# Kernel tuning notes

Hardware: AMD Instinct MI355X
Metric: run time of the kernel (lower is better)

## Reference

```python
import jax, jax.numpy as jnp
import numpy as np
from jax import lax

B, T, IN, H = 128, 1024, 130, 512


def setup_inputs() -> dict:
    key = jax.random.key(0)
    ks = jax.random.split(key, 6)
    inputs = jax.random.normal(ks[0], (B, T, IN), dtype=jnp.float32)
    # valid lengths in [1, T] (forward indexes outputs[len-1])
    inputs_len = jax.random.randint(ks[1], (B,), 1, T + 1)
    h0 = jnp.zeros((B, H), dtype=jnp.float32)
    c0 = jnp.zeros((B, H), dtype=jnp.float32)
    s = 1.0 / np.sqrt(H)
    W_ih = jax.random.uniform(ks[2], (4 * H, IN - 2), jnp.float32, -s, s)
    W_hh = jax.random.uniform(ks[3], (4 * H, H), jnp.float32, -s, s)
    b_ih = jax.random.uniform(ks[4], (4 * H,), jnp.float32, -s, s)
    b_hh = jax.random.uniform(ks[5], (4 * H,), jnp.float32, -s, s)
    return {"inputs": inputs, "inputs_len": inputs_len, "h0": h0, "c0": c0,
            "W_ih": W_ih, "W_hh": W_hh, "b_ih": b_ih, "b_hh": b_hh}


def _lstm_encode(inputs, h0, c0, W_ih, W_hh, b_ih, b_hh):
    # drop last 2 features (coordinates), as in stard_LSTM branch
    x = inputs[..., :-2]                                   # [B, T, IN-2]
    # precompute input projections for all timesteps (same math as per-step)
    xproj = jnp.einsum('bti,gi->tbg', x, W_ih) + b_ih + b_hh  # [T, B, 4H]

    def step(carry, xw):
        h, c = carry
        gates = xw + h @ W_hh.T                            # [B, 4H]
        i, f, g, o = jnp.split(gates, 4, axis=-1)
        i = jax.nn.sigmoid(i)
        f = jax.nn.sigmoid(f)
        g = jnp.tanh(g)
        o = jax.nn.sigmoid(o)
        c2 = f * c + i * g
        h2 = o * jnp.tanh(c2)
        return (h2, c2), h2

    _, hs = lax.scan(step, (h0, c0), xproj)                # hs: [T, B, H]
    return hs


def reference(inputs, inputs_len, h0, c0, W_ih, W_hh, b_ih, b_hh):
    hs = _lstm_encode(inputs, h0, c0, W_ih, W_hh, b_ih, b_hh)
    # gather hidden state at last valid timestep per sequence
    b_idx = jnp.arange(inputs.shape[0])
    return hs[inputs_len - 1, b_idx]                       # [B, H]
```

## Files before the change

### kernel.cpp

```cpp
#include <hip/hip_runtime.h>
#include <hip/hip_bf16.h>
#include <cstdint>
#include <cstddef>

#define T_STEPS 1024
#define BATCH   128
#define INF     128
#define HID     512
#define NBLK    256
#define NTHR    512
#define PK      648
#define Z_SHORTS    (2 * 16 * PK)
#define GSTR        17
#define GATE_FLOATS (4 * 4 * 16 * GSTR)
#define SMEM_BYTES  (Z_SHORTS * 2 + GATE_FLOATS * 4)

typedef short  bf16x8 __attribute__((ext_vector_type(8)));
typedef float  f32x4  __attribute__((ext_vector_type(4)));

static __device__ __forceinline__ unsigned short bf_hi(float v) {
  __hip_bfloat16 h = __float2bfloat16(v);
  return *reinterpret_cast<unsigned short*>(&h);
}
static __device__ __forceinline__ float bf_val(unsigned short u) {
  __hip_bfloat16 h = *reinterpret_cast<__hip_bfloat16*>(&u);
  return __bfloat162float(h);
}
static __device__ __forceinline__ float fsigmoid(float x) {
  return 1.f / (1.f + __expf(-x));
}
static __device__ __forceinline__ float ftanh(float x) {
  return 1.f - 2.f / (__expf(2.f * x) + 1.f);
}


__global__ __launch_bounds__(256) void k_prep_x(const float* __restrict__ in,
                                                unsigned short* __restrict__ xp)
{
  int t = blockIdx.x >> 3, bg = blockIdx.x & 7;
  int tid = threadIdx.x;
  size_t base = (size_t)blockIdx.x * 4096;
  #pragma unroll
  for (int rep = 0; rep < 8; ++rep) {
    int idx = rep * 256 + tid;
    int c = idx >> 7, k = idx & 127;
    float v = in[((size_t)(bg * 16 + c) * T_STEPS + t) * 130 + k];
    unsigned short hi = bf_hi(v);
    unsigned short lo = bf_hi(v - bf_val(hi));
    xp[base + c * 128 + k]        = hi;
    xp[base + 2048 + c * 128 + k] = lo;
  }
}

__global__ __launch_bounds__(64) void k_prep_w(const float* __restrict__ Wih,
                                               const float* __restrict__ Whh,
                                               unsigned short* __restrict__ wf)
{
  int blk = blockIdx.x;
  int s = blk % 5; int r = blk / 5;
  int kq = r & 3; int q = (r >> 2) & 3; int ug = r >> 4;
  int l = threadIdx.x;
  int Grow = q * HID + ug * 16 + (l & 15);
  int kb = kq * 160 + s * 32 + (l >> 4) * 8;
  float v[8];
  #pragma unroll
  for (int j = 0; j < 8; ++j)
    v[j] = (kb < INF) ? Wih[(size_t)Grow * INF + kb + j]
                      : Whh[(size_t)Grow * HID + (kb - INF) + j];
  unsigned short hi[8], lo[8];
  #pragma unroll
  for (int j = 0; j < 8; ++j) {
    hi[j] = bf_hi(v[j]);
    lo[j] = bf_hi(v[j] - bf_val(hi[j]));
  }
  unsigned short* dh = wf + ((size_t)(blk * 2 + 0) * 64 + l) * 8;
  unsigned short* dl = wf + ((size_t)(blk * 2 + 1) * 64 + l) * 8;
  #pragma unroll
  for (int j = 0; j < 8; ++j) { dh[j] = hi[j]; dl[j] = lo[j]; }
}

__global__ __launch_bounds__(256) void k_prep_h(const float* __restrict__ h0,
                                                unsigned* __restrict__ hp0,
                                                unsigned* __restrict__ flags)
{
  int idx = blockIdx.x * 256 + threadIdx.x;
  int k = idx & 511, c = (idx >> 9) & 15, bg = idx >> 13;
  float v = h0[(size_t)(bg * 16 + c) * HID + k];
  unsigned short hi = bf_hi(v);
  unsigned short lo = bf_hi(v - bf_val(hi));
  hp0[idx] = (unsigned)hi | ((unsigned)lo << 16);
  if (blockIdx.x == 0 && threadIdx.x < 256) flags[threadIdx.x] = 0;
}

__global__ __launch_bounds__(NTHR, 2) void k_persist(
    const unsigned short* __restrict__ xp,
    const unsigned short* __restrict__ wf,
    const float* __restrict__ bih, const float* __restrict__ bhh,
    unsigned* __restrict__ hp0,
    unsigned* __restrict__ hp1,
    const float* __restrict__ c0,
    const int* __restrict__ len,
    float* __restrict__ out,
    unsigned* __restrict__ flags)
{
  extern __shared__ char smem[];
  short* zpl   = (short*)smem;
  float* gates = (float*)(smem + Z_SHORTS * 2);

  const int blk = blockIdx.x;
  const int ug = blk & 31, bg = blk >> 5;
  const int tid = threadIdx.x;
  const int w = tid >> 6, l = tid & 63;
  const int kq = w & 3, th = w >> 2;
  const int cB = l & 15, gch = l >> 4;
  const int q0 = th * 2, q1 = th * 2 + 1;

  const uint4* wfq = (const uint4*)wf;
#define LDW(q_, s_, p_) \
  (*reinterpret_cast<const bf16x8*>(&wfq[(size_t)((((ug * 4 + (q_)) * 4 + kq) * 5 + (s_)) * 2 + (p_)) * 64 + l]))
  bf16x8 Aa0h = LDW(q0,0,0), Aa0l = LDW(q0,0,1), Aa1h = LDW(q0,1,0), Aa1l = LDW(q0,1,1);
  bf16x8 Aa2h = LDW(q0,2,0), Aa2l = LDW(q0,2,1), Aa3h = LDW(q0,3,0), Aa3l = LDW(q0,3,1);
  bf16x8 Aa4h = LDW(q0,4,0), Aa4l = LDW(q0,4,1);
  bf16x8 Ab0h = LDW(q1,0,0), Ab0l = LDW(q1,0,1), Ab1h = LDW(q1,1,0), Ab1l = LDW(q1,1,1);
  bf16x8 Ab2h = LDW(q1,2,0), Ab2l = LDW(q1,2,1), Ab3h = LDW(q1,3,0), Ab3l = LDW(q1,3,1);
  bf16x8 Ab4h = LDW(q1,4,0), Ab4l = LDW(q1,4,1);
#undef LDW
  asm volatile("" : "+v"(Aa0h), "+v"(Aa0l), "+v"(Aa1h), "+v"(Aa1l), "+v"(Aa2h),
                    "+v"(Aa2l), "+v"(Aa3h), "+v"(Aa3l), "+v"(Aa4h), "+v"(Aa4l),
                    "+v"(Ab0h), "+v"(Ab0l), "+v"(Ab1h), "+v"(Ab1l), "+v"(Ab2h),
                    "+v"(Ab2l), "+v"(Ab3h), "+v"(Ab3l), "+v"(Ab4h), "+v"(Ab4l));

  const int cb = tid & 15, cu = (tid >> 4) & 15;
  const int gb = bg * 16 + cb, hu = ug * 16 + cu;
  float c_reg = 0.f, bsq[4] = {0.f, 0.f, 0.f, 0.f};
  int mylen = -1;
  if (tid < 256) {
    c_reg = c0[(size_t)gb * HID + hu];
    mylen = len[gb];
    #pragma unroll
    for (int q = 0; q < 4; ++q) bsq[q] = bih[q * HID + hu] + bhh[q * HID + hu];
  }

  unsigned* myflags = flags + bg * 32;

  for (int t = 0; t < T_STEPS; ++t) {
    {
      const uint4* xps = (const uint4*)(xp + (size_t)(t * 8 + bg) * 4096);
      uint4 xa = xps[tid];
      int p = tid >> 8, c = (tid >> 4) & 15, kc = tid & 15;
      *(uint4*)(zpl + (p * 16 + c) * PK + kc * 8) = xa;
    }

    if (t) {
      if (tid < 32) {
        while (__hip_atomic_load(myflags + tid, __ATOMIC_RELAXED,
                                 __HIP_MEMORY_SCOPE_AGENT) < (unsigned)t)
          __builtin_amdgcn_s_sleep(1);
      }
      __syncthreads();
    }
    const unsigned* hsrc = ((t & 1) ? hp1 : hp0) + (size_t)bg * 8192;
    unsigned*       hdst = ((t & 1) ? hp0 : hp1) + (size_t)bg * 8192;

    unsigned long long hch[8];
    const unsigned long long* hq = (const unsigned long long*)hsrc;
    #pragma unroll
    for (int j = 0; j < 8; ++j)
      hch[j] = __hip_atomic_load(hq + j * 512 + tid, __ATOMIC_RELAXED,
                                 __HIP_MEMORY_SCOPE_AGENT);
    #pragma unroll
    for (int j = 0; j < 8; ++j) {
      int ci = j * 512 + tid;
      int c = ci >> 8, kp = ci & 255;
      unsigned w0 = (unsigned)hch[j], w1 = (unsigned)(hch[j] >> 32);
      unsigned hipair = (w0 & 0xFFFFu) | (w1 << 16);
      unsigned lopair = (w0 >> 16) | (w1 & 0xFFFF0000u);
      *(unsigned*)(zpl + c * PK + 128 + 2 * kp)        = hipair;
      *(unsigned*)(zpl + (16 + c) * PK + 128 + 2 * kp) = lopair;
    }
    __syncthreads();

    f32x4 acc0 = {0, 0, 0, 0}, acc1 = {0, 0, 0, 0};
#define KSTEP(s_, AH0, AL0, AH1, AL1)                                          \
  {                                                                            \
    int ka = kq * 160 + (s_) * 32 + gch * 8;                                   \
    bf16x8 Bh = *(const bf16x8*)(zpl + cB * PK + ka);                          \
    bf16x8 Bl = *(const bf16x8*)(zpl + (16 + cB) * PK + ka);                   \
    acc0 = __builtin_amdgcn_mfma_f32_16x16x32_bf16(AH0, Bh, acc0, 0, 0, 0);    \
    acc0 = __builtin_amdgcn_mfma_f32_16x16x32_bf16(AH0, Bl, acc0, 0, 0, 0);    \
    acc0 = __builtin_amdgcn_mfma_f32_16x16x32_bf16(AL0, Bh, acc0, 0, 0, 0);    \
    acc1 = __builtin_amdgcn_mfma_f32_16x16x32_bf16(AH1, Bh, acc1, 0, 0, 0);    \
    acc1 = __builtin_amdgcn_mfma_f32_16x16x32_bf16(AH1, Bl, acc1, 0, 0, 0);    \
    acc1 = __builtin_amdgcn_mfma_f32_16x16x32_bf16(AL1, Bh, acc1, 0, 0, 0);    \
  }
    KSTEP(0, Aa0h, Aa0l, Ab0h, Ab0l)
    KSTEP(1, Aa1h, Aa1l, Ab1h, Ab1l)
    KSTEP(2, Aa2h, Aa2l, Ab2h, Ab2l)
    KSTEP(3, Aa3h, Aa3l, Ab3h, Ab3l)
    KSTEP(4, Aa4h, Aa4l, Ab4h, Ab4l)
#undef KSTEP

    #pragma unroll
    for (int rr = 0; rr < 4; ++rr) {
      gates[((kq * 4 + q0) * 16 + gch * 4 + rr) * GSTR + cB] = acc0[rr];
      gates[((kq * 4 + q1) * 16 + gch * 4 + rr) * GSTR + cB] = acc1[rr];
    }
    __syncthreads();

    if (tid < 256) {
      float s4[4];
      #pragma unroll
      for (int q = 0; q < 4; ++q) {
        float s = bsq[q];
        #pragma unroll
        for (int kp = 0; kp < 4; ++kp)
          s += gates[((kp * 4 + q) * 16 + cu) * GSTR + cb];
        s4[q] = s;
      }
      float iv = fsigmoid(s4[0]);
      float fv = fsigmoid(s4[1]);
      float gv = ftanh(s4[2]);
      float ov = fsigmoid(s4[3]);
      c_reg = fv * c_reg + iv * gv;
      float h2 = ov * ftanh(c_reg);
      unsigned short hh = bf_hi(h2);
      unsigned short ll = bf_hi(h2 - bf_val(hh));
      __hip_atomic_store(hdst + (size_t)cb * 512 + hu,
                         (unsigned)hh | ((unsigned)ll << 16),
                         __ATOMIC_RELAXED, __HIP_MEMORY_SCOPE_AGENT);
      if (t == mylen - 1) out[(size_t)gb * HID + hu] = h2;
    }

    __syncthreads();
    if (tid == 0)
      __hip_atomic_store(myflags + ug, (unsigned)(t + 1),
                         __ATOMIC_RELAXED, __HIP_MEMORY_SCOPE_AGENT);
  }
}

extern "C" void kernel_launch(void* const* d_in, const int* in_sizes, int n_in,
                              void* d_out, int out_size, void* d_ws, size_t ws_size,
                              hipStream_t stream)
{
  const float* inputs = (const float*)d_in[0];
  const int*   len    = (const int*)  d_in[1];
  const float* h0     = (const float*)d_in[2];
  const float* c0     = (const float*)d_in[3];
  const float* Wih    = (const float*)d_in[4];
  const float* Whh    = (const float*)d_in[5];
  const float* bih    = (const float*)d_in[6];
  const float* bhh    = (const float*)d_in[7];
  float* out = (float*)d_out;

  char* p = (char*)d_ws;
  unsigned short* xp = (unsigned short*)p; p += (size_t)T_STEPS * 8 * 4096 * 2;
  unsigned short* wf = (unsigned short*)p; p += (size_t)2560 * 2 * 64 * 8 * 2;
  unsigned* hp0 = (unsigned*)p;  p += (size_t)8 * 16 * 512 * 4;
  unsigned* hp1 = (unsigned*)p;  p += (size_t)8 * 16 * 512 * 4;
  unsigned* flags = (unsigned*)p; p += 256 * 4;

  (void)hipFuncSetAttribute((const void*)k_persist,
                            hipFuncAttributeMaxDynamicSharedMemorySize, SMEM_BYTES);

  k_prep_x<<<T_STEPS * 8, 256, 0, stream>>>(inputs, xp);
  k_prep_w<<<2560, 64, 0, stream>>>(Wih, Whh, wf);
  k_prep_h<<<256, 256, 0, stream>>>(h0, hp0, flags);

  void* args[] = {(void*)&xp, (void*)&wf, (void*)&bih, (void*)&bhh,
                  (void*)&hp0, (void*)&hp1, (void*)&c0, (void*)&len,
                  (void*)&out, (void*)&flags};
  (void)hipLaunchCooperativeKernel((void*)k_persist, dim3(NBLK), dim3(NTHR),
                                   args, SMEM_BYTES, stream);
}
```

Before: 3.055 ms.

## Map batch groups to single XCD and use L2-scoped sync when co-located

```diff
diff --git a/kernel.cpp b/kernel.cpp
--- a/kernel.cpp
+++ b/kernel.cpp
@@ -90,6 +90,7 @@
   unsigned short lo = bf_hi(v - bf_val(hi));
   hp0[idx] = (unsigned)hi | ((unsigned)lo << 16);
   if (blockIdx.x == 0 && threadIdx.x < 256) flags[threadIdx.x] = 0;
+  if (blockIdx.x == 1 && threadIdx.x < 32)  flags[512 + threadIdx.x] = 0;
 }
 
 __global__ __launch_bounds__(NTHR, 2) void k_persist(
@@ -106,9 +107,10 @@
   extern __shared__ char smem[];
   short* zpl   = (short*)smem;
   float* gates = (float*)(smem + Z_SHORTS * 2);
+  __shared__ unsigned s_fast;
 
   const int blk = blockIdx.x;
-  const int ug = blk & 31, bg = blk >> 5;
+  const int bg = blk & 7, ug = blk >> 3;
   const int tid = threadIdx.x;
   const int w = tid >> 6, l = tid & 63;
   const int kq = w & 3, th = w >> 2;
@@ -142,6 +144,33 @@
   }
 
   unsigned* myflags = flags + bg * 32;
+  unsigned* xcds = flags + 256;
+  unsigned* ctr  = flags + 512;
+
+  unsigned myxcd;
+  asm volatile("s_getreg_b32 %0, hwreg(HW_REG_XCC_ID)" : "=s"(myxcd));
+  if (tid == 0) {
+    __hip_atomic_store(xcds + blk, myxcd, __ATOMIC_RELAXED, __HIP_MEMORY_SCOPE_AGENT);
+    asm volatile("s_waitcnt vmcnt(0)" ::: "memory");
+    __hip_atomic_fetch_add(ctr, 1u, __ATOMIC_RELAXED, __HIP_MEMORY_SCOPE_AGENT);
+    while (__hip_atomic_load(ctr, __ATOMIC_RELAXED, __HIP_MEMORY_SCOPE_AGENT) < NBLK)
+      __builtin_amdgcn_s_sleep(4);
+  }
+  __syncthreads();
+  {
+    unsigned ok = 1;
+    if (tid < 32) {
+      unsigned x = __hip_atomic_load(xcds + (tid * 8 + bg), __ATOMIC_RELAXED,
+                                     __HIP_MEMORY_SCOPE_AGENT);
+      ok = (x == myxcd) ? 1u : 0u;
+    }
+    if (tid < 64) {
+      unsigned long long m = __ballot(ok != 0);
+      if (tid == 0) s_fast = (m == ~0ull) ? 1u : 0u;
+    }
+  }
+  __syncthreads();
+  const bool fast = (s_fast != 0);
 
   for (int t = 0; t < T_STEPS; ++t) {
     {
@@ -153,9 +182,18 @@
 
     if (t) {
       if (tid < 32) {
-        while (__hip_atomic_load(myflags + tid, __ATOMIC_RELAXED,
-                                 __HIP_MEMORY_SCOPE_AGENT) < (unsigned)t)
-          __builtin_amdgcn_s_sleep(1);
+        const unsigned* fp = myflags + tid;
+        if (fast) {
+          unsigned v;
+          do {
+            asm volatile("global_load_dword %0, %1, off sc0\n\ts_waitcnt vmcnt(0)"
+                         : "=v"(v) : "v"(fp) : "memory");
+          } while (v < (unsigned)t);
+        } else {
+          while (__hip_atomic_load(fp, __ATOMIC_RELAXED,
+                                   __HIP_MEMORY_SCOPE_AGENT) < (unsigned)t)
+            __builtin_amdgcn_s_sleep(1);
+        }
       }
       __syncthreads();
     }
@@ -164,10 +202,16 @@
 
     unsigned long long hch[8];
     const unsigned long long* hq = (const unsigned long long*)hsrc;
-    #pragma unroll
-    for (int j = 0; j < 8; ++j)
-      hch[j] = __hip_atomic_load(hq + j * 512 + tid, __ATOMIC_RELAXED,
-                                 __HIP_MEMORY_SCOPE_AGENT);
+    if (fast) {
+      asm volatile("buffer_inv" ::: "memory");
+      #pragma unroll
+      for (int j = 0; j < 8; ++j) hch[j] = hq[j * 512 + tid];
+    } else {
+      #pragma unroll
+      for (int j = 0; j < 8; ++j)
+        hch[j] = __hip_atomic_load(hq + j * 512 + tid, __ATOMIC_RELAXED,
+                                   __HIP_MEMORY_SCOPE_AGENT);
+    }
     #pragma unroll
     for (int j = 0; j < 8; ++j) {
       int ci = j * 512 + tid;
@@ -225,16 +269,19 @@
       float h2 = ov * ftanh(c_reg);
       unsigned short hh = bf_hi(h2);
       unsigned short ll = bf_hi(h2 - bf_val(hh));
-      __hip_atomic_store(hdst + (size_t)cb * 512 + hu,
-                         (unsigned)hh | ((unsigned)ll << 16),
-                         __ATOMIC_RELAXED, __HIP_MEMORY_SCOPE_AGENT);
+      unsigned hv = (unsigned)hh | ((unsigned)ll << 16);
+      if (fast) hdst[(size_t)cb * 512 + hu] = hv;
+      else __hip_atomic_store(hdst + (size_t)cb * 512 + hu, hv,
+                              __ATOMIC_RELAXED, __HIP_MEMORY_SCOPE_AGENT);
       if (t == mylen - 1) out[(size_t)gb * HID + hu] = h2;
     }
 
     __syncthreads();
-    if (tid == 0)
-      __hip_atomic_store(myflags + ug, (unsigned)(t + 1),
-                         __ATOMIC_RELAXED, __HIP_MEMORY_SCOPE_AGENT);
+    if (tid == 0) {
+      if (fast) *(volatile unsigned*)(myflags + ug) = (unsigned)(t + 1);
+      else __hip_atomic_store(myflags + ug, (unsigned)(t + 1),
+                              __ATOMIC_RELAXED, __HIP_MEMORY_SCOPE_AGENT);
+    }
   }
 }
 
@@ -257,7 +304,7 @@
   unsigned short* wf = (unsigned short*)p; p += (size_t)2560 * 2 * 64 * 8 * 2;
   unsigned* hp0 = (unsigned*)p;  p += (size_t)8 * 16 * 512 * 4;
   unsigned* hp1 = (unsigned*)p;  p += (size_t)8 * 16 * 512 * 4;
-  unsigned* flags = (unsigned*)p; p += 256 * 4;
+  unsigned* flags = (unsigned*)p; p += 544 * 4;
 
   (void)hipFuncSetAttribute((const void*)k_persist,
                             hipFuncAttributeMaxDynamicSharedMemorySize, SMEM_BYTES);
```

After: 4.538 ms. 1.49x slower.

## Interleave two batch groups per block to hide recurrent sync latency

Applied to the files above, without the earlier changes.

```diff
diff --git a/kernel.cpp b/kernel.cpp
--- a/kernel.cpp
+++ b/kernel.cpp
@@ -7,13 +7,13 @@
 #define BATCH   128
 #define INF     128
 #define HID     512
-#define NBLK    256
+#define NBLK    128
 #define NTHR    512
 #define PK      648
 #define Z_SHORTS    (2 * 16 * PK)
 #define GSTR        17
 #define GATE_FLOATS (4 * 4 * 16 * GSTR)
-#define SMEM_BYTES  (Z_SHORTS * 2 + GATE_FLOATS * 4)
+#define SMEM_BYTES  (2 * Z_SHORTS * 2 + GATE_FLOATS * 4)
 
 typedef short  bf16x8 __attribute__((ext_vector_type(8)));
 typedef float  f32x4  __attribute__((ext_vector_type(4)));
@@ -104,11 +104,13 @@
     unsigned* __restrict__ flags)
 {
   extern __shared__ char smem[];
-  short* zpl   = (short*)smem;
-  float* gates = (float*)(smem + Z_SHORTS * 2);
+  short* zplA  = (short*)smem;
+  short* zplB  = zplA + Z_SHORTS;
+  float* gates = (float*)(smem + 2 * Z_SHORTS * 2);
 
   const int blk = blockIdx.x;
-  const int ug = blk & 31, bg = blk >> 5;
+  const int ug = blk & 31, pr = blk >> 5;
+  const int bgA = pr * 2, bgB = pr * 2 + 1;
   const int tid = threadIdx.x;
   const int w = tid >> 6, l = tid & 63;
   const int kq = w & 3, th = w >> 2;
@@ -131,61 +133,34 @@
                     "+v"(Ab2l), "+v"(Ab3h), "+v"(Ab3l), "+v"(Ab4h), "+v"(Ab4l));
 
   const int cb = tid & 15, cu = (tid >> 4) & 15;
-  const int gb = bg * 16 + cb, hu = ug * 16 + cu;
-  float c_reg = 0.f, bsq[4] = {0.f, 0.f, 0.f, 0.f};
-  int mylen = -1;
+  const int gbA = bgA * 16 + cb, gbB = bgB * 16 + cb;
+  const int hu = ug * 16 + cu;
+  float cA = 0.f, cBv = 0.f, bsq[4] = {0.f, 0.f, 0.f, 0.f};
+  int lenA = -1, lenB = -1;
   if (tid < 256) {
-    c_reg = c0[(size_t)gb * HID + hu];
-    mylen = len[gb];
+    cA  = c0[(size_t)gbA * HID + hu];
+    cBv = c0[(size_t)gbB * HID + hu];
+    lenA = len[gbA];
+    lenB = len[gbB];
     #pragma unroll
     for (int q = 0; q < 4; ++q) bsq[q] = bih[q * HID + hu] + bhh[q * HID + hu];
   }
 
-  unsigned* myflags = flags + bg * 32;
-
-  for (int t = 0; t < T_STEPS; ++t) {
-    {
-      const uint4* xps = (const uint4*)(xp + (size_t)(t * 8 + bg) * 4096);
-      uint4 xa = xps[tid];
-      int p = tid >> 8, c = (tid >> 4) & 15, kc = tid & 15;
-      *(uint4*)(zpl + (p * 16 + c) * PK + kc * 8) = xa;
-    }
-
-    if (t) {
-      if (tid < 32) {
-        while (__hip_atomic_load(myflags + tid, __ATOMIC_RELAXED,
-                                 __HIP_MEMORY_SCOPE_AGENT) < (unsigned)t)
-          __builtin_amdgcn_s_sleep(1);
-      }
-      __syncthreads();
-    }
-    const unsigned* hsrc = ((t & 1) ? hp1 : hp0) + (size_t)bg * 8192;
-    unsigned*       hdst = ((t & 1) ? hp0 : hp1) + (size_t)bg * 8192;
-
-    unsigned long long hch[8];
-    const unsigned long long* hq = (const unsigned long long*)hsrc;
-    #pragma unroll
-    for (int j = 0; j < 8; ++j)
-      hch[j] = __hip_atomic_load(hq + j * 512 + tid, __ATOMIC_RELAXED,
-                                 __HIP_MEMORY_SCOPE_AGENT);
-    #pragma unroll
-    for (int j = 0; j < 8; ++j) {
-      int ci = j * 512 + tid;
-      int c = ci >> 8, kp = ci & 255;
-      unsigned w0 = (unsigned)hch[j], w1 = (unsigned)(hch[j] >> 32);
-      unsigned hipair = (w0 & 0xFFFFu) | (w1 << 16);
-      unsigned lopair = (w0 >> 16) | (w1 & 0xFFFF0000u);
-      *(unsigned*)(zpl + c * PK + 128 + 2 * kp)        = hipair;
-      *(unsigned*)(zpl + (16 + c) * PK + 128 + 2 * kp) = lopair;
-    }
-    __syncthreads();
-
-    f32x4 acc0 = {0, 0, 0, 0}, acc1 = {0, 0, 0, 0};
-#define KSTEP(s_, AH0, AL0, AH1, AL1)                                          \
+  unsigned* flagsA = flags + bgA * 32;
+  unsigned* flagsB = flags + bgB * 32;
+
+  {
+    const uint4* xps = (const uint4*)(xp + (size_t)(0 * 8 + bgA) * 4096);
+    uint4 xa = xps[tid];
+    int p = tid >> 8, c = (tid >> 4) & 15, kc = tid & 15;
+    *(uint4*)(zplA + (p * 16 + c) * PK + kc * 8) = xa;
+  }
+
+#define KSTEP(ZP, s_, AH0, AL0, AH1, AL1)                                      \
   {                                                                            \
     int ka = kq * 160 + (s_) * 32 + gch * 8;                                   \
-    bf16x8 Bh = *(const bf16x8*)(zpl + cB * PK + ka);                          \
-    bf16x8 Bl = *(const bf16x8*)(zpl + (16 + cB) * PK + ka);                   \
+    bf16x8 Bh = *(const bf16x8*)((ZP) + cB * PK + ka);                         \
+    bf16x8 Bl = *(const bf16x8*)((ZP) + (16 + cB) * PK + ka);                  \
     acc0 = __builtin_amdgcn_mfma_f32_16x16x32_bf16(AH0, Bh, acc0, 0, 0, 0);    \
     acc0 = __builtin_amdgcn_mfma_f32_16x16x32_bf16(AH0, Bl, acc0, 0, 0, 0);    \
     acc0 = __builtin_amdgcn_mfma_f32_16x16x32_bf16(AL0, Bh, acc0, 0, 0, 0);    \
@@ -193,49 +168,93 @@
     acc1 = __builtin_amdgcn_mfma_f32_16x16x32_bf16(AH1, Bl, acc1, 0, 0, 0);    \
     acc1 = __builtin_amdgcn_mfma_f32_16x16x32_bf16(AL1, Bh, acc1, 0, 0, 0);    \
   }
-    KSTEP(0, Aa0h, Aa0l, Ab0h, Ab0l)
-    KSTEP(1, Aa1h, Aa1l, Ab1h, Ab1l)
-    KSTEP(2, Aa2h, Aa2l, Ab2h, Ab2l)
-    KSTEP(3, Aa3h, Aa3l, Ab3h, Ab3l)
-    KSTEP(4, Aa4h, Aa4l, Ab4h, Ab4l)
+
+#define PHASE(FLG, HSRC, HDST, ZSELF, ZOTHER, XOIDX, CREG, MYLEN, GB)          \
+  {                                                                            \
+    if (t) {                                                                   \
+      if (tid < 32) {                                                          \
+        const unsigned* fp = (FLG) + tid;                                      \
+        while (__hip_atomic_load(fp, __ATOMIC_RELAXED,                         \
+                                 __HIP_MEMORY_SCOPE_AGENT) < (unsigned)t)      \
+          __builtin_amdgcn_s_sleep(1);                                         \
+      }                                                                        \
+    }                                                                          \
+    __syncthreads();                                                           \
+    unsigned long long hch[8];                                                 \
+    const unsigned long long* hq = (const unsigned long long*)(HSRC);          \
+    _Pragma("unroll")                                                          \
+    for (int j = 0; j < 8; ++j)                                                \
+      hch[j] = __hip_atomic_load(hq + j * 512 + tid, __ATOMIC_RELAXED,         \
+                                 __HIP_MEMORY_SCOPE_AGENT);                    \
+    uint4 xo = ((const uint4*)(xp + (size_t)(XOIDX) * 4096))[tid];             \
+    _Pragma("unroll")                                                          \
+    for (int j = 0; j < 8; ++j) {                                              \
+      int ci = j * 512 + tid;                                                  \
+      int c = ci >> 8, kp = ci & 255;                                          \
+      unsigned w0 = (unsigned)hch[j], w1 = (unsigned)(hch[j] >> 32);           \
+      unsigned hipair = (w0 & 0xFFFFu) | (w1 << 16);                           \
+      unsigned lopair = (w0 >> 16) | (w1 & 0xFFFF0000u);                       \
+      *(unsigned*)((ZSELF) + c * PK + 128 + 2 * kp)        = hipair;           \
+      *(unsigned*)((ZSELF) + (16 + c) * PK + 128 + 2 * kp) = lopair;           \
+    }                                                                          \
+    {                                                                          \
+      int p = tid >> 8, c = (tid >> 4) & 15, kc = tid & 15;                    \
+      *(uint4*)((ZOTHER) + (p * 16 + c) * PK + kc * 8) = xo;                   \
+    }                                                                          \
+    __syncthreads();                                                           \
+    f32x4 acc0 = {0, 0, 0, 0}, acc1 = {0, 0, 0, 0};                            \
+    KSTEP(ZSELF, 0, Aa0h, Aa0l, Ab0h, Ab0l)                                    \
+    KSTEP(ZSELF, 1, Aa1h, Aa1l, Ab1h, Ab1l)                                    \
+    KSTEP(ZSELF, 2, Aa2h, Aa2l, Ab2h, Ab2l)                                    \
+    KSTEP(ZSELF, 3, Aa3h, Aa3l, Ab3h, Ab3l)                                    \
+    KSTEP(ZSELF, 4, Aa4h, Aa4l, Ab4h, Ab4l)                                    \
+    _Pragma("unroll")                                                          \
+    for (int rr = 0; rr < 4; ++rr) {                                           \
+      gates[((kq * 4 + q0) * 16 + gch * 4 + rr) * GSTR + cB] = acc0[rr];       \
+      gates[((kq * 4 + q1) * 16 + gch * 4 + rr) * GSTR + cB] = acc1[rr];       \
+    }                                                                          \
+    __syncthreads();                                                           \
+    if (tid < 256) {                                                           \
+      float s4[4];                                                             \
+      _Pragma("unroll")                                                        \
+      for (int q = 0; q < 4; ++q) {                                            \
+        float s = bsq[q];                                                      \
+        _Pragma("unroll")                                                      \
+        for (int kp = 0; kp < 4; ++kp)                                         \
+          s += gates[((kp * 4 + q) * 16 + cu) * GSTR + cb];                    \
+        s4[q] = s;                                                             \
+      }                                                                        \
+      float iv = fsigmoid(s4[0]);                                              \
+      float fv = fsigmoid(s4[1]);                                              \
+      float gv = ftanh(s4[2]);                                                 \
+      float ov = fsigmoid(s4[3]);                                              \
+      (CREG) = fv * (CREG) + iv * gv;                                          \
+      float h2 = ov * ftanh(CREG);                                             \
+      unsigned short hh = bf_hi(h2);                                           \
+      unsigned short ll = bf_hi(h2 - bf_val(hh));                              \
+      __hip_atomic_store((HDST) + (size_t)cb * 512 + hu,                       \
+                         (unsigned)hh | ((unsigned)ll << 16),                  \
+                         __ATOMIC_RELAXED, __HIP_MEMORY_SCOPE_AGENT);          \
+      if (t == (MYLEN) - 1) out[(size_t)(GB) * HID + hu] = h2;                 \
+    }                                                                          \
+    __syncthreads();         \
+    if (tid == 0)                                                              \
+      __hip_atomic_store((FLG) + ug, (unsigned)(t + 1),                        \
+                         __ATOMIC_RELAXED, __HIP_MEMORY_SCOPE_AGENT);          \
+  }
+
+  for (int t = 0; t < T_STEPS; ++t) {
+    const unsigned* hsA = ((t & 1) ? hp1 : hp0) + (size_t)bgA * 8192;
+    unsigned*       hdA = ((t & 1) ? hp0 : hp1) + (size_t)bgA * 8192;
+    const unsigned* hsB = ((t & 1) ? hp1 : hp0) + (size_t)bgB * 8192;
+    unsigned*       hdB = ((t & 1) ? hp0 : hp1) + (size_t)bgB * 8192;
+    const int tn = (t + 1 < T_STEPS) ? t + 1 : t;
+
+    PHASE(flagsA, hsA, hdA, zplA, zplB, t * 8 + bgB, cA, lenA, gbA)
+    PHASE(flagsB, hsB, hdB, zplB, zplA, tn * 8 + bgA, cBv, lenB, gbB)
+  }
+#undef PHASE
 #undef KSTEP
-
-    #pragma unroll
-    for (int rr = 0; rr < 4; ++rr) {
-      gates[((kq * 4 + q0) * 16 + gch * 4 + rr) * GSTR + cB] = acc0[rr];
-      gates[((kq * 4 + q1) * 16 + gch * 4 + rr) * GSTR + cB] = acc1[rr];
-    }
-    __syncthreads();
-
-    if (tid < 256) {
-      float s4[4];
-      #pragma unroll
-      for (int q = 0; q < 4; ++q) {
-        float s = bsq[q];
-        #pragma unroll
-        for (int kp = 0; kp < 4; ++kp)
-          s += gates[((kp * 4 + q) * 16 + cu) * GSTR + cb];
-        s4[q] = s;
-      }
-      float iv = fsigmoid(s4[0]);
-      float fv = fsigmoid(s4[1]);
-      float gv = ftanh(s4[2]);
-      float ov = fsigmoid(s4[3]);
-      c_reg = fv * c_reg + iv * gv;
-      float h2 = ov * ftanh(c_reg);
-      unsigned short hh = bf_hi(h2);
-      unsigned short ll = bf_hi(h2 - bf_val(hh));
-      __hip_atomic_store(hdst + (size_t)cb * 512 + hu,
-                         (unsigned)hh | ((unsigned)ll << 16),
-                         __ATOMIC_RELAXED, __HIP_MEMORY_SCOPE_AGENT);
-      if (t == mylen - 1) out[(size_t)gb * HID + hu] = h2;
-    }
-
-    __syncthreads();
-    if (tid == 0)
-      __hip_atomic_store(myflags + ug, (unsigned)(t + 1),
-                         __ATOMIC_RELAXED, __HIP_MEMORY_SCOPE_AGENT);
-  }
 }
 
 extern "C" void kernel_launch(void* const* d_in, const int* in_sizes, int n_in,
```

Measured after the change: 4.951 ms. +62.1%, slower.

## Replace per-block flag barrier with timestamped h words and gate-interleaved MFMA layout

Applied to the files above, without the earlier changes.

```diff
diff --git a/kernel.cpp b/kernel.cpp
--- a/kernel.cpp
+++ b/kernel.cpp
@@ -11,9 +11,9 @@
 #define NTHR    512
 #define PK      648
 #define Z_SHORTS    (2 * 16 * PK)
-#define GSTR        17
-#define GATE_FLOATS (4 * 4 * 16 * GSTR)
-#define SMEM_BYTES  (Z_SHORTS * 2 + GATE_FLOATS * 4)
+#define Z_BYTES     (Z_SHORTS * 2)
+#define RED_BYTES   (256 * 16)
+#define SMEM_BYTES  (2 * Z_BYTES + RED_BYTES)
 
 typedef short  bf16x8 __attribute__((ext_vector_type(8)));
 typedef float  f32x4  __attribute__((ext_vector_type(4)));
@@ -57,11 +57,12 @@
                                                unsigned short* __restrict__ wf)
 {
   int blk = blockIdx.x;
-  int s = blk % 5; int r = blk / 5;
-  int kq = r & 3; int q = (r >> 2) & 3; int ug = r >> 4;
+  int s = blk % 10; int r = blk / 10;
+  int kh = r & 1; int u4 = (r >> 1) & 3; int ug = r >> 3;
   int l = threadIdx.x;
-  int Grow = q * HID + ug * 16 + (l & 15);
-  int kb = kq * 160 + s * 32 + (l >> 4) * 8;
+  int m = l & 15;
+  int Grow = (m & 3) * HID + ug * 16 + u4 * 4 + (m >> 2);
+  int kb = kh * 320 + s * 32 + (l >> 4) * 8;
   float v[8];
   #pragma unroll
   for (int j = 0; j < 8; ++j)
@@ -80,161 +81,149 @@
 }
 
 __global__ __launch_bounds__(256) void k_prep_h(const float* __restrict__ h0,
-                                                unsigned* __restrict__ hp0,
-                                                unsigned* __restrict__ flags)
+                                                unsigned long long* __restrict__ hp0)
 {
   int idx = blockIdx.x * 256 + threadIdx.x;
-  int k = idx & 511, c = (idx >> 9) & 15, bg = idx >> 13;
-  float v = h0[(size_t)(bg * 16 + c) * HID + k];
+  int bg = idx >> 13;
+  int r = idx & 8191;
+  int u = r >> 4, c = r & 15;
+  float v = h0[(size_t)(bg * 16 + c) * HID + u];
   unsigned short hi = bf_hi(v);
   unsigned short lo = bf_hi(v - bf_val(hi));
-  hp0[idx] = (unsigned)hi | ((unsigned)lo << 16);
-  if (blockIdx.x == 0 && threadIdx.x < 256) flags[threadIdx.x] = 0;
+  hp0[idx] = (unsigned long long)((unsigned)hi | ((unsigned)lo << 16));
 }
 
 __global__ __launch_bounds__(NTHR, 2) void k_persist(
     const unsigned short* __restrict__ xp,
     const unsigned short* __restrict__ wf,
     const float* __restrict__ bih, const float* __restrict__ bhh,
-    unsigned* __restrict__ hp0,
-    unsigned* __restrict__ hp1,
+    unsigned long long* __restrict__ hp0,
+    unsigned long long* __restrict__ hp1,
     const float* __restrict__ c0,
     const int* __restrict__ len,
-    float* __restrict__ out,
-    unsigned* __restrict__ flags)
+    float* __restrict__ out)
 {
   extern __shared__ char smem[];
-  short* zpl   = (short*)smem;
-  float* gates = (float*)(smem + Z_SHORTS * 2);
+  short* zpl = (short*)smem;
+  f32x4* red = (f32x4*)(smem + 2 * Z_BYTES);
 
   const int blk = blockIdx.x;
   const int ug = blk & 31, bg = blk >> 5;
   const int tid = threadIdx.x;
   const int w = tid >> 6, l = tid & 63;
-  const int kq = w & 3, th = w >> 2;
+  const int u4 = w & 3, kh = w >> 2;
   const int cB = l & 15, gch = l >> 4;
-  const int q0 = th * 2, q1 = th * 2 + 1;
 
   const uint4* wfq = (const uint4*)wf;
-#define LDW(q_, s_, p_) \
-  (*reinterpret_cast<const bf16x8*>(&wfq[(size_t)((((ug * 4 + (q_)) * 4 + kq) * 5 + (s_)) * 2 + (p_)) * 64 + l]))
-  bf16x8 Aa0h = LDW(q0,0,0), Aa0l = LDW(q0,0,1), Aa1h = LDW(q0,1,0), Aa1l = LDW(q0,1,1);
-  bf16x8 Aa2h = LDW(q0,2,0), Aa2l = LDW(q0,2,1), Aa3h = LDW(q0,3,0), Aa3l = LDW(q0,3,1);
-  bf16x8 Aa4h = LDW(q0,4,0), Aa4l = LDW(q0,4,1);
-  bf16x8 Ab0h = LDW(q1,0,0), Ab0l = LDW(q1,0,1), Ab1h = LDW(q1,1,0), Ab1l = LDW(q1,1,1);
-  bf16x8 Ab2h = LDW(q1,2,0), Ab2l = LDW(q1,2,1), Ab3h = LDW(q1,3,0), Ab3l = LDW(q1,3,1);
-  bf16x8 Ab4h = LDW(q1,4,0), Ab4l = LDW(q1,4,1);
+  const int fbase = ((ug * 4 + u4) * 2 + kh) * 10;
+#define LDW(s_, p_) \
+  (*reinterpret_cast<const bf16x8*>(&wfq[(size_t)((fbase + (s_)) * 2 + (p_)) * 64 + l]))
+  bf16x8 A0h = LDW(0,0), A0l = LDW(0,1), A1h = LDW(1,0), A1l = LDW(1,1);
+  bf16x8 A2h = LDW(2,0), A2l = LDW(2,1), A3h = LDW(3,0), A3l = LDW(3,1);
+  bf16x8 A4h = LDW(4,0), A4l = LDW(4,1), A5h = LDW(5,0), A5l = LDW(5,1);
+  bf16x8 A6h = LDW(6,0), A6l = LDW(6,1), A7h = LDW(7,0), A7l = LDW(7,1);
+  bf16x8 A8h = LDW(8,0), A8l = LDW(8,1), A9h = LDW(9,0), A9l = LDW(9,1);
 #undef LDW
-  asm volatile("" : "+v"(Aa0h), "+v"(Aa0l), "+v"(Aa1h), "+v"(Aa1l), "+v"(Aa2h),
-                    "+v"(Aa2l), "+v"(Aa3h), "+v"(Aa3l), "+v"(Aa4h), "+v"(Aa4l),
-                    "+v"(Ab0h), "+v"(Ab0l), "+v"(Ab1h), "+v"(Ab1l), "+v"(Ab2h),
-                    "+v"(Ab2l), "+v"(Ab3h), "+v"(Ab3l), "+v"(Ab4h), "+v"(Ab4l));
-
-  const int cb = tid & 15, cu = (tid >> 4) & 15;
-  const int gb = bg * 16 + cb, hu = ug * 16 + cu;
+  asm volatile("" : "+v"(A0h), "+v"(A0l), "+v"(A1h), "+v"(A1l), "+v"(A2h),
+                    "+v"(A2l), "+v"(A3h), "+v"(A3l), "+v"(A4h), "+v"(A4l),
+                    "+v"(A5h), "+v"(A5l), "+v"(A6h), "+v"(A6l), "+v"(A7h),
+                    "+v"(A7l), "+v"(A8h), "+v"(A8l), "+v"(A9h), "+v"(A9l));
+
+  const int cb = l & 15;
+  const int hu = ug * 16 + u4 * 4 + (l >> 4);
+  const int gb = bg * 16 + cb;
   float c_reg = 0.f, bsq[4] = {0.f, 0.f, 0.f, 0.f};
   int mylen = -1;
   if (tid < 256) {
     c_reg = c0[(size_t)gb * HID + hu];
     mylen = len[gb];
     #pragma unroll
-    for (int q = 0; q < 4; ++q) bsq[q] = bih[q * HID + hu] + bhh[q * HID + hu];
-  }
-
-  unsigned* myflags = flags + bg * 32;
+    for (int g = 0; g < 4; ++g) bsq[g] = bih[g * HID + hu] + bhh[g * HID + hu];
+  }
+
+  const int pc = tid & 15, qq = tid >> 4;
+  const int pbase = 32 * qq + pc;
 
   for (int t = 0; t < T_STEPS; ++t) {
+    short* zcur = zpl + (t & 1) * Z_SHORTS;
+    const unsigned long long* hq = ((t & 1) ? hp1 : hp0) + (size_t)bg * 8192;
+    unsigned long long*       hd = ((t & 1) ? hp0 : hp1) + (size_t)bg * 8192;
+
+    uint4 xv = ((const uint4*)(xp + (size_t)(t * 8 + bg) * 4096))[tid];
+
+    unsigned long long hch[16];
+    #pragma unroll
+    for (int j = 0; j < 16; ++j)
+      hch[j] = __hip_atomic_load(hq + 1024 * (j >> 1) + 16 * (j & 1) + pbase,
+                                 __ATOMIC_RELAXED, __HIP_MEMORY_SCOPE_AGENT);
+    for (;;) {
+      int bad = 0;
+      #pragma unroll
+      for (int j = 0; j < 16; ++j)
+        if ((unsigned)(hch[j] >> 32) != (unsigned)t) {
+          hch[j] = __hip_atomic_load(hq + 1024 * (j >> 1) + 16 * (j & 1) + pbase,
+                                     __ATOMIC_RELAXED, __HIP_MEMORY_SCOPE_AGENT);
+          bad = 1;
+        }
+      if (!__any(bad)) break;
+      __builtin_amdgcn_s_sleep(1);
+    }
+
     {
-      const uint4* xps = (const uint4*)(xp + (size_t)(t * 8 + bg) * 4096);
-      uint4 xa = xps[tid];
-      int p = tid >> 8, c = (tid >> 4) & 15, kc = tid & 15;
-      *(uint4*)(zpl + (p * 16 + c) * PK + kc * 8) = xa;
-    }
-
-    if (t) {
-      if (tid < 32) {
-        while (__hip_atomic_load(myflags + tid, __ATOMIC_RELAXED,
-                                 __HIP_MEMORY_SCOPE_AGENT) < (unsigned)t)
-          __builtin_amdgcn_s_sleep(1);
-      }
-      __syncthreads();
-    }
-    const unsigned* hsrc = ((t & 1) ? hp1 : hp0) + (size_t)bg * 8192;
-    unsigned*       hdst = ((t & 1) ? hp0 : hp1) + (size_t)bg * 8192;
-
-    unsigned long long hch[8];
-    const unsigned long long* hq = (const unsigned long long*)hsrc;
+      int p_ = tid >> 8, c_ = (tid >> 4) & 15, kc = tid & 15;
+      *(uint4*)(zcur + (p_ * 16 + c_) * PK + kc * 8) = xv;
+    }
     #pragma unroll
-    for (int j = 0; j < 8; ++j)
-      hch[j] = __hip_atomic_load(hq + j * 512 + tid, __ATOMIC_RELAXED,
-                                 __HIP_MEMORY_SCOPE_AGENT);
-    #pragma unroll
-    for (int j = 0; j < 8; ++j) {
-      int ci = j * 512 + tid;
-      int c = ci >> 8, kp = ci & 255;
-      unsigned w0 = (unsigned)hch[j], w1 = (unsigned)(hch[j] >> 32);
-      unsigned hipair = (w0 & 0xFFFFu) | (w1 << 16);
-      unsigned lopair = (w0 >> 16) | (w1 & 0xFFFF0000u);
-      *(unsigned*)(zpl + c * PK + 128 + 2 * kp)        = hipair;
-      *(unsigned*)(zpl + (16 + c) * PK + 128 + 2 * kp) = lopair;
+    for (int p = 0; p < 8; ++p) {
+      unsigned e0 = (unsigned)hch[2 * p], e1 = (unsigned)hch[2 * p + 1];
+      unsigned hipair = (e0 & 0xFFFFu) | (e1 << 16);
+      unsigned lopair = (e0 >> 16) | (e1 & 0xFFFF0000u);
+      int off = pc * PK + 128 + 64 * p + 2 * qq;
+      *(unsigned*)(zcur + off)           = hipair;
+      *(unsigned*)(zcur + 16 * PK + off) = lopair;
     }
     __syncthreads();
 
-    f32x4 acc0 = {0, 0, 0, 0}, acc1 = {0, 0, 0, 0};
-#define KSTEP(s_, AH0, AL0, AH1, AL1)                                          \
+    f32x4 accE = {0, 0, 0, 0}, accO = {0, 0, 0, 0};
+#define KSTEP(s_, AH, AL, ACC)                                                 \
   {                                                                            \
-    int ka = kq * 160 + (s_) * 32 + gch * 8;                                   \
-    bf16x8 Bh = *(const bf16x8*)(zpl + cB * PK + ka);                          \
-    bf16x8 Bl = *(const bf16x8*)(zpl + (16 + cB) * PK + ka);                   \
-    acc0 = __builtin_amdgcn_mfma_f32_16x16x32_bf16(AH0, Bh, acc0, 0, 0, 0);    \
-    acc0 = __builtin_amdgcn_mfma_f32_16x16x32_bf16(AH0, Bl, acc0, 0, 0, 0);    \
-    acc0 = __builtin_amdgcn_mfma_f32_16x16x32_bf16(AL0, Bh, acc0, 0, 0, 0);    \
-    acc1 = __builtin_amdgcn_mfma_f32_16x16x32_bf16(AH1, Bh, acc1, 0, 0, 0);    \
-    acc1 = __builtin_amdgcn_mfma_f32_16x16x32_bf16(AH1, Bl, acc1, 0, 0, 0);    \
-    acc1 = __builtin_amdgcn_mfma_f32_16x16x32_bf16(AL1, Bh, acc1, 0, 0, 0);    \
-  }
-    KSTEP(0, Aa0h, Aa0l, Ab0h, Ab0l)
-    KSTEP(1, Aa1h, Aa1l, Ab1h, Ab1l)
-    KSTEP(2, Aa2h, Aa2l, Ab2h, Ab2l)
-    KSTEP(3, Aa3h, Aa3l, Ab3h, Ab3l)
-    KSTEP(4, Aa4h, Aa4l, Ab4h, Ab4l)
+    int ka = kh * 320 + (s_) * 32 + gch * 8;                                   \
+    bf16x8 Bh = *(const bf16x8*)(zcur + cB * PK + ka);                         \
+    bf16x8 Bl = *(const bf16x8*)(zcur + 16 * PK + cB * PK + ka);               \
+    ACC = __builtin_amdgcn_mfma_f32_16x16x32_bf16(AH, Bh, ACC, 0, 0, 0);       \
+    ACC = __builtin_amdgcn_mfma_f32_16x16x32_bf16(AH, Bl, ACC, 0, 0, 0);       \
+    ACC = __builtin_amdgcn_mfma_f32_16x16x32_bf16(AL, Bh, ACC, 0, 0, 0);       \
+  }
+    KSTEP(0, A0h, A0l, accE) KSTEP(1, A1h, A1l, accO)
+    KSTEP(2, A2h, A2l, accE) KSTEP(3, A3h, A3l, accO)
+    KSTEP(4, A4h, A4l, accE) KSTEP(5, A5h, A5l, accO)
+    KSTEP(6, A6h, A6l, accE) KSTEP(7, A7h, A7l, accO)
+    KSTEP(8, A8h, A8l, accE) KSTEP(9, A9h, A9l, accO)
 #undef KSTEP
-
-    #pragma unroll
-    for (int rr = 0; rr < 4; ++rr) {
-      gates[((kq * 4 + q0) * 16 + gch * 4 + rr) * GSTR + cB] = acc0[rr];
-      gates[((kq * 4 + q1) * 16 + gch * 4 + rr) * GSTR + cB] = acc1[rr];
-    }
+    f32x4 acc = accE + accO;
+
+    if (w >= 4) red[u4 * 64 + l] = acc;
     __syncthreads();
-
     if (tid < 256) {
-      float s4[4];
-      #pragma unroll
-      for (int q = 0; q < 4; ++q) {
-        float s = bsq[q];
-        #pragma unroll
-        for (int kp = 0; kp < 4; ++kp)
-          s += gates[((kp * 4 + q) * 16 + cu) * GSTR + cb];
-        s4[q] = s;
-      }
-      float iv = fsigmoid(s4[0]);
-      float fv = fsigmoid(s4[1]);
-      float gv = ftanh(s4[2]);
-      float ov = fsigmoid(s4[3]);
+      f32x4 o = red[u4 * 64 + l];
+      float s0 = acc[0] + o[0] + bsq[0];
+      float s1 = acc[1] + o[1] + bsq[1];
+      float s2 = acc[2] + o[2] + bsq[2];
+      float s3 = acc[3] + o[3] + bsq[3];
+      float iv = fsigmoid(s0);
+      float fv = fsigmoid(s1);
+      float gv = ftanh(s2);
+      float ov = fsigmoid(s3);
       c_reg = fv * c_reg + iv * gv;
       float h2 = ov * ftanh(c_reg);
       unsigned short hh = bf_hi(h2);
       unsigned short ll = bf_hi(h2 - bf_val(hh));
-      __hip_atomic_store(hdst + (size_t)cb * 512 + hu,
-                         (unsigned)hh | ((unsigned)ll << 16),
+      unsigned long long word = ((unsigned long long)(unsigned)(t + 1) << 32)
+                              | (unsigned long long)((unsigned)hh | ((unsigned)ll << 16));
+      __hip_atomic_store(hd + hu * 16 + cb, word,
                          __ATOMIC_RELAXED, __HIP_MEMORY_SCOPE_AGENT);
       if (t == mylen - 1) out[(size_t)gb * HID + hu] = h2;
     }
-
-    __syncthreads();
-    if (tid == 0)
-      __hip_atomic_store(myflags + ug, (unsigned)(t + 1),
-                         __ATOMIC_RELAXED, __HIP_MEMORY_SCOPE_AGENT);
   }
 }
 
@@ -255,20 +244,19 @@
   char* p = (char*)d_ws;
   unsigned short* xp = (unsigned short*)p; p += (size_t)T_STEPS * 8 * 4096 * 2;
   unsigned short* wf = (unsigned short*)p; p += (size_t)2560 * 2 * 64 * 8 * 2;
-  unsigned* hp0 = (unsigned*)p;  p += (size_t)8 * 16 * 512 * 4;
-  unsigned* hp1 = (unsigned*)p;  p += (size_t)8 * 16 * 512 * 4;
-  unsigned* flags = (unsigned*)p; p += 256 * 4;
+  unsigned long long* hp0 = (unsigned long long*)p; p += (size_t)8 * 8192 * 8;
+  unsigned long long* hp1 = (unsigned long long*)p; p += (size_t)8 * 8192 * 8;
 
   (void)hipFuncSetAttribute((const void*)k_persist,
                             hipFuncAttributeMaxDynamicSharedMemorySize, SMEM_BYTES);
 
   k_prep_x<<<T_STEPS * 8, 256, 0, stream>>>(inputs, xp);
   k_prep_w<<<2560, 64, 0, stream>>>(Wih, Whh, wf);
-  k_prep_h<<<256, 256, 0, stream>>>(h0, hp0, flags);
+  k_prep_h<<<256, 256, 0, stream>>>(h0, hp0);
 
   void* args[] = {(void*)&xp, (void*)&wf, (void*)&bih, (void*)&bhh,
                   (void*)&hp0, (void*)&hp1, (void*)&c0, (void*)&len,
-                  (void*)&out, (void*)&flags};
+                  (void*)&out};
   (void)hipLaunchCooperativeKernel((void*)k_persist, dim3(NBLK), dim3(NTHR),
                                    args, SMEM_BYTES, stream);
 }
```

After: 3.774 ms. 23.6% more time.
